# Kernel optimization log

Measured on AMD Instinct MI355X. Metric: run time of the kernel, lower is better.

Reference implementation:

```python
import jax, jax.numpy as jnp
import numpy as np

B, S, E, H, A, D, V, L = 64, 196, 512, 512, 256, 512, 32000, 32
PAD_IDX = 2


def setup_inputs() -> dict:
    key = jax.random.key(0)
    ks = jax.random.split(key, 20)
    sc = 0.02
    return {
        "encoder_out": jax.random.normal(ks[0], (B, S, E), jnp.float32),
        "pooled": jax.random.normal(ks[1], (B, E), jnp.float32),
        "targets": jax.random.randint(ks[2], (B, L), 0, V, jnp.int64),
        "embedding": jax.random.normal(ks[3], (V, D), jnp.float32) * sc,
        "W_enc": jax.random.normal(ks[4], (A, E), jnp.float32) * sc,
        "b_enc": jnp.zeros((A,), jnp.float32),
        "W_dec": jax.random.normal(ks[5], (A, H), jnp.float32) * sc,
        "b_dec": jnp.zeros((A,), jnp.float32),
        "W_score": jax.random.normal(ks[6], (1, A), jnp.float32) * sc,
        "b_score": jnp.zeros((1,), jnp.float32),
        "W_ih": jax.random.normal(ks[7], (3 * H, D + E), jnp.float32) * sc,
        "W_hh": jax.random.normal(ks[8], (3 * H, H), jnp.float32) * sc,
        "b_ih": jnp.zeros((3 * H,), jnp.float32),
        "b_hh": jnp.zeros((3 * H,), jnp.float32),
        "W_out": jax.random.normal(ks[9], (V, H), jnp.float32) * sc,
        "b_out": jnp.zeros((V,), jnp.float32),
        "W_init": jax.random.normal(ks[10], (H, E), jnp.float32) * sc,
        "b_init": jnp.zeros((H,), jnp.float32),
    }


def reference(encoder_out, pooled, targets, embedding, W_enc, b_enc, W_dec,
              b_dec, W_score, b_score, W_ih, W_hh, b_ih, b_hh, W_out, b_out,
              W_init, b_init):
    # padding_idx=2: that embedding row is zero
    emb_tab = embedding.at[PAD_IDX].set(0.0)
    # initial hidden state from pooled features
    h0 = jnp.tanh(pooled @ W_init.T + b_init)              # (B, H)
    # encoder projection is step-invariant; hoist out of the loop
    enc_proj = jnp.einsum('bse,ae->bsa', encoder_out, W_enc) + b_enc  # (B,S,A)
    # teacher forcing (ratio=1.0): inputs are targets[:, :-1]
    tokens = targets[:, :-1].T                              # (L-1, B)

    def step(h, tok):
        embedded = emb_tab[tok]                             # (B, D)
        # Bahdanau attention
        dec_proj = h @ W_dec.T + b_dec                      # (B, A)
        energy = jnp.tanh(enc_proj + dec_proj[:, None, :])  # (B, S, A)
        scores = jnp.einsum('bsa,a->bs', energy, W_score[0]) + b_score[0]
        weights = jax.nn.softmax(scores, axis=1)            # (B, S)
        context = jnp.einsum('bs,bse->be', weights, encoder_out)  # (B, E)
        # GRU cell (PyTorch gate ordering: r, z, n)
        x = jnp.concatenate([embedded, context], axis=1)    # (B, D+E)
        gi = x @ W_ih.T + b_ih                              # (B, 3H)
        gh = h @ W_hh.T + b_hh                              # (B, 3H)
        gi_r, gi_z, gi_n = jnp.split(gi, 3, axis=1)
        gh_r, gh_z, gh_n = jnp.split(gh, 3, axis=1)
        r = jax.nn.sigmoid(gi_r + gh_r)
        z = jax.nn.sigmoid(gi_z + gh_z)
        n = jnp.tanh(gi_n + r * gh_n)
        h_new = (1.0 - z) * n + z * h
        logits = h_new @ W_out.T + b_out                    # (B, V)
        return h_new, logits

    _, logits = jax.lax.scan(step, h0, tokens)              # (L-1, B, V)
    return jnp.transpose(logits, (1, 0, 2))                 # (B, L-1, V)
```

## Files before the change

### kernel.cpp

```cpp
#include <hip/hip_runtime.h>

using bf16x8 = __attribute__((ext_vector_type(8))) short;
using f32x4  = __attribute__((ext_vector_type(4))) float;

__device__ inline float bf2f(unsigned short h){
  union { unsigned int u; float f; } v; v.u = ((unsigned int)h) << 16; return v.f;
}
__device__ inline unsigned short f2b(float x){
  union { float f; unsigned int u; } v; v.f = x;
  unsigned int r = (v.u + 0x7FFFu + ((v.u >> 16) & 1u)) >> 16;
  return (unsigned short)r;
}
__device__ inline float blo(unsigned int u){ union{unsigned int v; float f;} t; t.v = u << 16; return t.f; }
__device__ inline float bhi(unsigned int u){ union{unsigned int v; float f;} t; t.v = u & 0xffff0000u; return t.f; }

__global__ void conv_k(const float* __restrict__ s, unsigned short* __restrict__ d, int n){
  int i = (blockIdx.x * 256 + threadIdx.x) * 4;
  if (i >= n) return;
  float4 v = *(const float4*)(s + i);
  unsigned int p0 = (unsigned int)f2b(v.x) | ((unsigned int)f2b(v.y) << 16);
  unsigned int p1 = (unsigned int)f2b(v.z) | ((unsigned int)f2b(v.w) << 16);
  *(uint2*)(d + i) = make_uint2(p0, p1);
}

__global__ void wdect_k(const float* __restrict__ Wd, unsigned short* __restrict__ o){
  int idx = blockIdx.x * 256 + threadIdx.x;
  int k = idx >> 8, a = idx & 255;
  o[idx] = f2b(Wd[a * 512 + k]);
}

__global__ void embed_k(const int* __restrict__ tgt, const float* __restrict__ emb,
                        unsigned short* __restrict__ out, int n){
  int idx = blockIdx.x * 256 + threadIdx.x;
  if (idx >= n) return;
  int d = idx & 511, m = idx >> 9, t = m >> 6, b = m & 63;
  int tok = tgt[b * 32 + t];
  float v = (tok == 2) ? 0.f : emb[(long)tok * 512 + d];
  out[idx] = f2b(v);
}

#define EPI_PLAIN 0
#define EPI_TANH  1
#define EPI_OUT   2
#define EPI_B16   3

template<int EPI, bool AF32>
__global__ __launch_bounds__(256)
void gemm_bt(const void* __restrict__ Av, int lda,
             const unsigned short* __restrict__ Bp, int ldb,
             const float* __restrict__ bias,
             float* __restrict__ Cf, unsigned short* __restrict__ Cb, int ldc,
             int K,
             int n_split, const void* __restrict__ A2v,
             const unsigned short* __restrict__ B2p, int lda2, int ldb2)
{
  __shared__ __align__(16) unsigned short As[64][40];
  __shared__ __align__(16) unsigned short Bs[256][40];

  int m0 = blockIdx.x * 64;
  int n0 = blockIdx.y * 256;
  const void* Ap = Av; const unsigned short* Bq = Bp;
  int la = lda, lb = ldb, nB = n0;
  if (n_split > 0 && n0 >= n_split){ Ap = A2v; Bq = B2p; la = lda2; lb = ldb2; nB = n0 - n_split; }

  int tid  = threadIdx.x;
  int wave = tid >> 6, lane = tid & 63, quad = lane >> 4, lrow = lane & 15;

  f32x4 acc[4][4];
#pragma unroll
  for (int i = 0; i < 4; ++i)
#pragma unroll
    for (int j = 0; j < 4; ++j)
#pragma unroll
      for (int r = 0; r < 4; ++r) acc[i][j][r] = 0.f;

  int ar = tid >> 2, ac = (tid & 3) * 8;

  for (int k0 = 0; k0 < K; k0 += 32){
    if (AF32){
      const float* A32 = (const float*)Ap;
      const float4* src = (const float4*)(A32 + (long)(m0 + ar) * la + k0 + ac);
      float4 x0 = src[0], x1 = src[1];
      unsigned int p0 = (unsigned int)f2b(x0.x) | ((unsigned int)f2b(x0.y) << 16);
      unsigned int p1 = (unsigned int)f2b(x0.z) | ((unsigned int)f2b(x0.w) << 16);
      unsigned int p2 = (unsigned int)f2b(x1.x) | ((unsigned int)f2b(x1.y) << 16);
      unsigned int p3 = (unsigned int)f2b(x1.z) | ((unsigned int)f2b(x1.w) << 16);
      *(uint4*)&As[ar][ac] = make_uint4(p0, p1, p2, p3);
    } else {
      const unsigned short* A16 = (const unsigned short*)Ap;
      *(uint4*)&As[ar][ac] = *(const uint4*)(A16 + (long)(m0 + ar) * la + k0 + ac);
    }
#pragma unroll
    for (int c = 0; c < 4; ++c){
      int id = tid + c * 256; int br = id >> 2, bc = (id & 3) * 8;
      *(uint4*)&Bs[br][bc] = *(const uint4*)(Bq + (long)(nB + br) * lb + k0 + bc);
    }
    __syncthreads();

    bf16x8 af[4], bfr[4];
#pragma unroll
    for (int mf = 0; mf < 4; ++mf) af[mf]  = *(const bf16x8*)&As[mf * 16 + lrow][quad * 8];
#pragma unroll
    for (int nf = 0; nf < 4; ++nf) bfr[nf] = *(const bf16x8*)&Bs[wave * 64 + nf * 16 + lrow][quad * 8];
#pragma unroll
    for (int mf = 0; mf < 4; ++mf)
#pragma unroll
      for (int nf = 0; nf < 4; ++nf)
        acc[mf][nf] = __builtin_amdgcn_mfma_f32_16x16x32_bf16(af[mf], bfr[nf], acc[mf][nf], 0, 0, 0);
    __syncthreads();
  }

#pragma unroll
  for (int mf = 0; mf < 4; ++mf){
#pragma unroll
    for (int nf = 0; nf < 4; ++nf){
#pragma unroll
      for (int r = 0; r < 4; ++r){
        int m = m0 + mf * 16 + quad * 4 + r;
        int n = n0 + wave * 64 + nf * 16 + lrow;
        float v = acc[mf][nf][r];
        if (bias) v += bias[n];
        if (EPI == EPI_TANH){
          v = tanhf(v);
          Cf[(long)m * ldc + n] = v;
          Cb[(long)m * ldc + n] = f2b(v);
        } else if (EPI == EPI_OUT){
          Cf[(long)(m & 63) * (31 * 32000) + (long)(m >> 6) * 32000 + n] = v;
        } else if (EPI == EPI_B16){
          Cb[(long)m * ldc + n] = f2b(v);
        } else {
          Cf[(long)m * ldc + n] = v;
        }
      }
    }
  }
}

__global__ __launch_bounds__(512)
void attn_step(const uint4* __restrict__ ep4,
               const unsigned int* __restrict__ eo2,
               const float* __restrict__ W_score,
               const float* __restrict__ b_dec,
               const float* __restrict__ b_hh,
               const float* __restrict__ gi_emb,
               const float* __restrict__ giq,
               float* __restrict__ h_all,
               unsigned short* __restrict__ h_b16,
               const uint2* __restrict__ WdecT4,
               unsigned short* __restrict__ ctx_b16,
               int t, int do_gates, int do_attn)
{
  __shared__ __align__(16) uint4 ep_s4[6272];
  __shared__ float sh_h[512];
  __shared__ float2 dpw[256];
  __shared__ float spart[2048];
  __shared__ float sw[256];
  __shared__ float wred[16];

  int b = blockIdx.x, tid = threadIdx.x;
  int lane = tid & 63, wv = tid >> 6;

  float hv;
  if (do_gates){
    int j = tid;
    long ge = ((long)(t - 1) * 64 + b) * 1536;
    long gq = (long)b * 3072;
    float gir = gi_emb[ge + j]        + giq[gq + j];
    float giz = gi_emb[ge + 512 + j]  + giq[gq + 512 + j];
    float gin = gi_emb[ge + 1024 + j] + giq[gq + 1024 + j];
    float ghr = giq[gq + 1536 + j]        + b_hh[j];
    float ghz = giq[gq + 1536 + 512 + j]  + b_hh[512 + j];
    float ghn = giq[gq + 1536 + 1024 + j] + b_hh[1024 + j];
    float rr = 1.f / (1.f + __expf(-(gir + ghr)));
    float zz = 1.f / (1.f + __expf(-(giz + ghz)));
    float nn = tanhf(gin + rr * ghn);
    float hp = h_all[((long)(t - 1) * 64 + b) * 512 + j];
    hv = (1.f - zz) * nn + zz * hp;
    h_all[((long)t * 64 + b) * 512 + j] = hv;
    h_b16[((long)t * 64 + b) * 512 + j] = f2b(hv);
  } else {
    hv = h_all[((long)t * 64 + b) * 512 + tid];
  }
  if (!do_attn) return;

  sh_h[tid] = hv;
  float wsc = (tid < 256) ? W_score[tid] : 0.f;

  {
    const uint4* src = ep4 + (long)b * 6272;
    for (int c = tid; c < 6272; c += 512){
      int r = c >> 5, col = c & 31;
      ep_s4[(r << 5) | (col ^ (r & 7))] = src[c];
    }
  }
  __syncthreads();

  {
    int a4 = tid & 63, kg = tid >> 6;
    const uint2* wp = WdecT4 + ((kg << 12) | a4);
    const float* hp = &sh_h[kg << 6];
    float ac0 = 0.f, ac1 = 0.f, ac2 = 0.f, ac3 = 0.f;
#pragma unroll 16
    for (int kk = 0; kk < 64; ++kk){
      uint2 wq = wp[kk << 6];
      float hk = hp[kk];
      ac0 += hk * blo(wq.x); ac1 += hk * bhi(wq.x);
      ac2 += hk * blo(wq.y); ac3 += hk * bhi(wq.y);
    }
    *(float4*)&spart[(kg << 8) | (a4 << 2)] = make_float4(ac0, ac1, ac2, ac3);
  }
  __syncthreads();
  if (tid < 256){
    float dp = b_dec[tid];
#pragma unroll
    for (int kg = 0; kg < 8; ++kg) dp += spart[(kg << 8) | tid];
    dpw[tid] = make_float2(dp, wsc);
  }
  __syncthreads();

  {
    int s = tid & 255, half = tid >> 8;
    float acc = 0.f;
    if (s < 196){
      int rb = s << 5, sx = s & 7;
#pragma unroll 4
      for (int j = 0; j < 16; ++j){
        uint4 v = ep_s4[rb | (((half << 4) | j) ^ sx)];
        int aj = (half << 7) | (j << 3);
#define SCP(uu, ab) { \
        float2 dA = dpw[ab], dB = dpw[(ab) + 1]; \
        float xA = blo(uu) + dA.x, xB = bhi(uu) + dB.x; \
        float eA = __expf(2.f * xA), eB = __expf(2.f * xB); \
        acc += dA.y * (1.f - 2.f / (eA + 1.f)); \
        acc += dB.y * (1.f - 2.f / (eB + 1.f)); }
        SCP(v.x, aj) SCP(v.y, aj + 2) SCP(v.z, aj + 4) SCP(v.w, aj + 6)
#undef SCP
      }
    }
    spart[tid] = acc;
  }
  __syncthreads();

  float sc = -1e30f, ee = 0.f;
  if (tid < 256) sc = (tid < 196) ? (spart[tid] + spart[tid + 256]) : -1e30f;
  float mm = sc;
#pragma unroll
  for (int off = 32; off >= 1; off >>= 1) mm = fmaxf(mm, __shfl_xor(mm, off));
  if (tid < 256 && lane == 0) wred[wv] = mm;
  __syncthreads();
  float mx = fmaxf(fmaxf(wred[0], wred[1]), fmaxf(wred[2], wred[3]));
  if (tid < 256){
    ee = (tid < 196) ? __expf(sc - mx) : 0.f;
    sw[tid] = ee;
  }
  float ss = ee;
#pragma unroll
  for (int off = 32; off >= 1; off >>= 1) ss += __shfl_xor(ss, off);
  if (tid < 256 && lane == 0) wred[8 + wv] = ss;
  __syncthreads();
  float inv = 1.f / (wred[8] + wred[9] + wred[10] + wred[11]);

  {
    int e2 = tid & 255, sh2 = tid >> 8;
    const unsigned int* src = eo2 + ((long)b * 196 + sh2 * 98) * 256 + e2;
    float a0 = 0.f, a1 = 0.f;
#pragma unroll 2
    for (int s2 = 0; s2 < 98; ++s2){
      unsigned int v = src[(long)s2 * 256];
      float w = sw[sh2 * 98 + s2];
      a0 += w * blo(v); a1 += w * bhi(v);
    }
    *(float2*)&spart[(sh2 << 9) | (e2 << 1)] = make_float2(a0, a1);
  }
  __syncthreads();
  {
    float cv = (spart[tid] + spart[tid + 512]) * inv;
    ctx_b16[(b << 9) | tid] = f2b(cv);
  }
}

extern "C" void kernel_launch(void* const* d_in, const int* in_sizes, int n_in,
                              void* d_out, int out_size, void* d_ws, size_t ws_size,
                              hipStream_t stream)
{
  (void)in_sizes; (void)n_in; (void)out_size; (void)ws_size;
  const float* encoder_out = (const float*)d_in[0];
  const float* pooled      = (const float*)d_in[1];
  const int*   targets     = (const int*)d_in[2];
  const float* embedding   = (const float*)d_in[3];
  const float* W_enc  = (const float*)d_in[4];
  const float* b_enc  = (const float*)d_in[5];
  const float* W_dec  = (const float*)d_in[6];
  const float* b_dec  = (const float*)d_in[7];
  const float* W_score= (const float*)d_in[8];
  const float* W_ih   = (const float*)d_in[10];
  const float* W_hh   = (const float*)d_in[11];
  const float* b_ih   = (const float*)d_in[12];
  const float* b_hh   = (const float*)d_in[13];
  const float* W_out  = (const float*)d_in[14];
  const float* b_out  = (const float*)d_in[15];
  const float* W_init = (const float*)d_in[16];
  const float* b_init = (const float*)d_in[17];
  float* out = (float*)d_out;

  char* w = (char*)d_ws;
  unsigned short* eo_b16  = (unsigned short*)w; w += 12845056;
  float* gi_emb           = (float*)w;          w += 12189696;
  float* h_all            = (float*)w;          w += 4194304;
  unsigned short* h_b16   = (unsigned short*)w; w += 2097152;
  float* giq              = (float*)w;          w += 786432;
  unsigned short* ctx_b16 = (unsigned short*)w; w += 65536;
  unsigned short* emb_b16 = (unsigned short*)w; w += 2031616;
  unsigned short* Wout_b  = (unsigned short*)w; w += 32768000;
  unsigned short* Wih_b   = (unsigned short*)w; w += 3145728;
  unsigned short* Whh_b   = (unsigned short*)w; w += 1572864;
  unsigned short* WdecT_b = (unsigned short*)w; w += 262144;
  unsigned short* Winit_b = (unsigned short*)w; w += 524288;
  unsigned short* Wenc_b  = (unsigned short*)w; w += 262144;
  unsigned short* ep_b16  = (unsigned short*)w; w += 6422528;

  auto conv = [&](const float* s, unsigned short* d, int n){
    conv_k<<<dim3((n / 4 + 255) / 256), dim3(256), 0, stream>>>(s, d, n);
  };
  conv(W_out,  Wout_b,  32000 * 512);
  conv(W_ih,   Wih_b,   1536 * 1024);
  conv(W_hh,   Whh_b,   1536 * 512);
  conv(W_init, Winit_b, 512 * 512);
  conv(W_enc,  Wenc_b,  256 * 512);
  conv(encoder_out, eo_b16, 64 * 196 * 512);
  wdect_k<<<dim3(512), dim3(256), 0, stream>>>(W_dec, WdecT_b);
  embed_k<<<dim3((1984 * 512) / 256), dim3(256), 0, stream>>>(targets, embedding, emb_b16, 1984 * 512);

  gemm_bt<EPI_TANH, true><<<dim3(1, 2), 256, 0, stream>>>(
      pooled, 512, Winit_b, 512, b_init, h_all, h_b16, 512, 512, 0, nullptr, nullptr, 0, 0);
  gemm_bt<EPI_B16, true><<<dim3(196, 1), 256, 0, stream>>>(
      encoder_out, 512, Wenc_b, 512, b_enc, nullptr, ep_b16, 256, 512, 0, nullptr, nullptr, 0, 0);
  gemm_bt<EPI_PLAIN, false><<<dim3(31, 6), 256, 0, stream>>>(
      emb_b16, 512, Wih_b, 1024, b_ih, gi_emb, nullptr, 1536, 512, 0, nullptr, nullptr, 0, 0);

  for (int t = 0; t < 31; ++t){
    attn_step<<<dim3(64), dim3(512), 0, stream>>>(
        (const uint4*)ep_b16, (const unsigned int*)eo_b16, W_score, b_dec, b_hh,
        gi_emb, giq, h_all, h_b16, (const uint2*)WdecT_b, ctx_b16,
        t, (t > 0) ? 1 : 0, 1);
    gemm_bt<EPI_PLAIN, false><<<dim3(1, 12), 256, 0, stream>>>(
        ctx_b16, 512, Wih_b + 512, 1024, nullptr, giq, nullptr, 3072, 512,
        1536, h_b16 + (long)t * 64 * 512, Whh_b, 512, 512);
  }
  attn_step<<<dim3(64), dim3(512), 0, stream>>>(
      (const uint4*)ep_b16, (const unsigned int*)eo_b16, W_score, b_dec, b_hh,
      gi_emb, giq, h_all, h_b16, (const uint2*)WdecT_b, ctx_b16, 31, 1, 0);

  gemm_bt<EPI_OUT, false><<<dim3(31, 125), 256, 0, stream>>>(
      h_b16 + 64 * 512, 512, Wout_b, 512, b_out, out, nullptr, 0, 512,
      0, nullptr, nullptr, 0, 0);
}
```

Before: 2.167 ms.

## Fuse recurrent GRU loop into one persistent per-batch kernel with MFMA gate GEMV

The 31 per-step attention launches plus per-step gate GEMM launches are replaced by a single persistent kernel with one block per batch row that loops over all time steps. Encoder projections stay in LDS, and the GRU hidden state and gate pre-activations are kept on chip. The ctx·W_ih and h·W_hh products are computed inside the block with MFMA 16x16x32 bf16 instructions, using weights pre-swizzled into fragment order by a new wfrag kernel. This removes about 62 launches and the global round trips between them. The cost is that only 64 blocks run, and each block now streams the full 3 MB of gate weights every step while the MFMA A operand is padded from one row to sixteen.

```diff
diff --git a/kernel.cpp b/kernel.cpp
--- a/kernel.cpp
+++ b/kernel.cpp
@@ -27,6 +27,15 @@
   int idx = blockIdx.x * 256 + threadIdx.x;
   int k = idx >> 8, a = idx & 255;
   o[idx] = f2b(Wd[a * 512 + k]);
+}
+
+__global__ void wfrag_k(const float* __restrict__ src, int ld, int koff,
+                        unsigned short* __restrict__ dst){
+  int d = blockIdx.x * 256 + threadIdx.x;
+  int j = d & 7, lane = (d >> 3) & 63, kit = (d >> 9) & 15, nt = d >> 13;
+  int n = nt * 16 + (lane & 15);
+  int k = kit * 32 + ((lane >> 4) << 3) + j;
+  dst[d] = f2b(src[(long)n * ld + koff + k]);
 }
 
 __global__ void embed_k(const int* __restrict__ tgt, const float* __restrict__ emb,
@@ -137,54 +146,34 @@
 }
 
 __global__ __launch_bounds__(512)
-void attn_step(const uint4* __restrict__ ep4,
-               const unsigned int* __restrict__ eo2,
-               const float* __restrict__ W_score,
-               const float* __restrict__ b_dec,
-               const float* __restrict__ b_hh,
-               const float* __restrict__ gi_emb,
-               const float* __restrict__ giq,
-               float* __restrict__ h_all,
-               unsigned short* __restrict__ h_b16,
-               const uint2* __restrict__ WdecT4,
-               unsigned short* __restrict__ ctx_b16,
-               int t, int do_gates, int do_attn)
+void loop_k(const uint4* __restrict__ ep4,
+            const unsigned int* __restrict__ eo2,
+            const float* __restrict__ W_score,
+            const float* __restrict__ b_dec,
+            const float* __restrict__ b_hh,
+            const float* __restrict__ gi_emb,
+            const float* __restrict__ h0_all,
+            unsigned short* __restrict__ h_b16,
+            const uint2* __restrict__ WdecT4,
+            const unsigned short* __restrict__ Wihf,
+            const unsigned short* __restrict__ Whhf)
 {
   __shared__ __align__(16) uint4 ep_s4[6272];
   __shared__ float sh_h[512];
+  __shared__ unsigned short sh_hb[512];
+  __shared__ unsigned short sh_cb[512];
   __shared__ float2 dpw[256];
   __shared__ float spart[2048];
   __shared__ float sw[256];
   __shared__ float wred[16];
+  __shared__ float giq_lds[3072];
 
   int b = blockIdx.x, tid = threadIdx.x;
-  int lane = tid & 63, wv = tid >> 6;
-
-  float hv;
-  if (do_gates){
-    int j = tid;
-    long ge = ((long)(t - 1) * 64 + b) * 1536;
-    long gq = (long)b * 3072;
-    float gir = gi_emb[ge + j]        + giq[gq + j];
-    float giz = gi_emb[ge + 512 + j]  + giq[gq + 512 + j];
-    float gin = gi_emb[ge + 1024 + j] + giq[gq + 1024 + j];
-    float ghr = giq[gq + 1536 + j]        + b_hh[j];
-    float ghz = giq[gq + 1536 + 512 + j]  + b_hh[512 + j];
-    float ghn = giq[gq + 1536 + 1024 + j] + b_hh[1024 + j];
-    float rr = 1.f / (1.f + __expf(-(gir + ghr)));
-    float zz = 1.f / (1.f + __expf(-(giz + ghz)));
-    float nn = tanhf(gin + rr * ghn);
-    float hp = h_all[((long)(t - 1) * 64 + b) * 512 + j];
-    hv = (1.f - zz) * nn + zz * hp;
-    h_all[((long)t * 64 + b) * 512 + j] = hv;
-    h_b16[((long)t * 64 + b) * 512 + j] = f2b(hv);
-  } else {
-    hv = h_all[((long)t * 64 + b) * 512 + tid];
-  }
-  if (!do_attn) return;
-
-  sh_h[tid] = hv;
-  float wsc = (tid < 256) ? W_score[tid] : 0.f;
+  int lane = tid & 63, wv = tid >> 6, quad = lane >> 4, lrow = lane & 15;
+
+  float wsc  = (tid < 256) ? W_score[tid] : 0.f;
+  float bdec = (tid < 256) ? b_dec[tid] : 0.f;
+  float bhh0 = b_hh[tid], bhh1 = b_hh[512 + tid], bhh2 = b_hh[1024 + tid];
 
   {
     const uint4* src = ep4 + (long)b * 6272;
@@ -193,89 +182,142 @@
       ep_s4[(r << 5) | (col ^ (r & 7))] = src[c];
     }
   }
-  __syncthreads();
-
-  {
-    int a4 = tid & 63, kg = tid >> 6;
-    const uint2* wp = WdecT4 + ((kg << 12) | a4);
-    const float* hp = &sh_h[kg << 6];
-    float ac0 = 0.f, ac1 = 0.f, ac2 = 0.f, ac3 = 0.f;
+
+  float h_prev = 0.f;
+
+  for (int t = 0; t <= 31; ++t){
+    float hv;
+    if (t > 0){
+      int j = tid;
+      long ge = ((long)(t - 1) * 64 + b) * 1536;
+      float gir = gi_emb[ge + j]        + giq_lds[j];
+      float giz = gi_emb[ge + 512 + j]  + giq_lds[512 + j];
+      float gin = gi_emb[ge + 1024 + j] + giq_lds[1024 + j];
+      float ghr = giq_lds[1536 + j] + bhh0;
+      float ghz = giq_lds[2048 + j] + bhh1;
+      float ghn = giq_lds[2560 + j] + bhh2;
+      float rr = 1.f / (1.f + __expf(-(gir + ghr)));
+      float zz = 1.f / (1.f + __expf(-(giz + ghz)));
+      float nn = tanhf(gin + rr * ghn);
+      hv = (1.f - zz) * nn + zz * h_prev;
+      h_b16[((long)t * 64 + b) * 512 + j] = f2b(hv);
+    } else {
+      hv = h0_all[(long)b * 512 + tid];
+    }
+    h_prev = hv;
+    if (t == 31) break;
+
+    sh_h[tid] = hv;
+    sh_hb[tid] = f2b(hv);
+    __syncthreads();
+
+    {
+      int a4 = tid & 63, kg = tid >> 6;
+      const uint2* wp = WdecT4 + ((kg << 12) | a4);
+      const float* hp = &sh_h[kg << 6];
+      float ac0 = 0.f, ac1 = 0.f, ac2 = 0.f, ac3 = 0.f;
 #pragma unroll 16
-    for (int kk = 0; kk < 64; ++kk){
-      uint2 wq = wp[kk << 6];
-      float hk = hp[kk];
-      ac0 += hk * blo(wq.x); ac1 += hk * bhi(wq.x);
-      ac2 += hk * blo(wq.y); ac3 += hk * bhi(wq.y);
-    }
-    *(float4*)&spart[(kg << 8) | (a4 << 2)] = make_float4(ac0, ac1, ac2, ac3);
-  }
-  __syncthreads();
-  if (tid < 256){
-    float dp = b_dec[tid];
-#pragma unroll
-    for (int kg = 0; kg < 8; ++kg) dp += spart[(kg << 8) | tid];
-    dpw[tid] = make_float2(dp, wsc);
-  }
-  __syncthreads();
-
-  {
-    int s = tid & 255, half = tid >> 8;
-    float acc = 0.f;
-    if (s < 196){
-      int rb = s << 5, sx = s & 7;
+      for (int kk = 0; kk < 64; ++kk){
+        uint2 wq = wp[kk << 6];
+        float hk = hp[kk];
+        ac0 += hk * blo(wq.x); ac1 += hk * bhi(wq.x);
+        ac2 += hk * blo(wq.y); ac3 += hk * bhi(wq.y);
+      }
+      *(float4*)&spart[(kg << 8) | (a4 << 2)] = make_float4(ac0, ac1, ac2, ac3);
+    }
+    __syncthreads();
+    if (tid < 256){
+      float dp = bdec;
+#pragma unroll
+      for (int kg = 0; kg < 8; ++kg) dp += spart[(kg << 8) | tid];
+      dpw[tid] = make_float2(dp, wsc);
+    }
+    __syncthreads();
+
+    {
+      int s = tid & 255, half = tid >> 8;
+      float acc = 0.f;
+      if (s < 196){
+        int rb = s << 5, sx = s & 7;
 #pragma unroll 4
-      for (int j = 0; j < 16; ++j){
-        uint4 v = ep_s4[rb | (((half << 4) | j) ^ sx)];
-        int aj = (half << 7) | (j << 3);
+        for (int j = 0; j < 16; ++j){
+          uint4 v = ep_s4[rb | (((half << 4) | j) ^ sx)];
+          int aj = (half << 7) | (j << 3);
 #define SCP(uu, ab) { \
-        float2 dA = dpw[ab], dB = dpw[(ab) + 1]; \
-        float xA = blo(uu) + dA.x, xB = bhi(uu) + dB.x; \
-        float eA = __expf(2.f * xA), eB = __expf(2.f * xB); \
-        acc += dA.y * (1.f - 2.f / (eA + 1.f)); \
-        acc += dB.y * (1.f - 2.f / (eB + 1.f)); }
-        SCP(v.x, aj) SCP(v.y, aj + 2) SCP(v.z, aj + 4) SCP(v.w, aj + 6)
+          float2 dA = dpw[ab], dB = dpw[(ab) + 1]; \
+          float xA = blo(uu) + dA.x, xB = bhi(uu) + dB.x; \
+          float eA = __expf(2.f * xA), eB = __expf(2.f * xB); \
+          acc += dA.y * (1.f - 2.f / (eA + 1.f)); \
+          acc += dB.y * (1.f - 2.f / (eB + 1.f)); }
+          SCP(v.x, aj) SCP(v.y, aj + 2) SCP(v.z, aj + 4) SCP(v.w, aj + 6)
 #undef SCP
-      }
-    }
-    spart[tid] = acc;
-  }
-  __syncthreads();
-
-  float sc = -1e30f, ee = 0.f;
-  if (tid < 256) sc = (tid < 196) ? (spart[tid] + spart[tid + 256]) : -1e30f;
-  float mm = sc;
-#pragma unroll
-  for (int off = 32; off >= 1; off >>= 1) mm = fmaxf(mm, __shfl_xor(mm, off));
-  if (tid < 256 && lane == 0) wred[wv] = mm;
-  __syncthreads();
-  float mx = fmaxf(fmaxf(wred[0], wred[1]), fmaxf(wred[2], wred[3]));
-  if (tid < 256){
-    ee = (tid < 196) ? __expf(sc - mx) : 0.f;
-    sw[tid] = ee;
-  }
-  float ss = ee;
-#pragma unroll
-  for (int off = 32; off >= 1; off >>= 1) ss += __shfl_xor(ss, off);
-  if (tid < 256 && lane == 0) wred[8 + wv] = ss;
-  __syncthreads();
-  float inv = 1.f / (wred[8] + wred[9] + wred[10] + wred[11]);
-
-  {
-    int e2 = tid & 255, sh2 = tid >> 8;
-    const unsigned int* src = eo2 + ((long)b * 196 + sh2 * 98) * 256 + e2;
-    float a0 = 0.f, a1 = 0.f;
+        }
+      }
+      spart[tid] = acc;
+    }
+    __syncthreads();
+
+    float sc = -1e30f, ee = 0.f;
+    if (tid < 256) sc = (tid < 196) ? (spart[tid] + spart[tid + 256]) : -1e30f;
+    float mm = sc;
+#pragma unroll
+    for (int off = 32; off >= 1; off >>= 1) mm = fmaxf(mm, __shfl_xor(mm, off));
+    if (tid < 256 && lane == 0) wred[wv] = mm;
+    __syncthreads();
+    float mx = fmaxf(fmaxf(wred[0], wred[1]), fmaxf(wred[2], wred[3]));
+    if (tid < 256){
+      ee = (tid < 196) ? __expf(sc - mx) : 0.f;
+      sw[tid] = ee;
+    }
+    float ss = ee;
+#pragma unroll
+    for (int off = 32; off >= 1; off >>= 1) ss += __shfl_xor(ss, off);
+    if (tid < 256 && lane == 0) wred[8 + wv] = ss;
+    __syncthreads();
+    float inv = 1.f / (wred[8] + wred[9] + wred[10] + wred[11]);
+
+    {
+      int e2 = tid & 255, sh2 = tid >> 8;
+      const unsigned int* src = eo2 + ((long)b * 196 + sh2 * 98) * 256 + e2;
+      float a0 = 0.f, a1 = 0.f;
 #pragma unroll 2
-    for (int s2 = 0; s2 < 98; ++s2){
-      unsigned int v = src[(long)s2 * 256];
-      float w = sw[sh2 * 98 + s2];
-      a0 += w * blo(v); a1 += w * bhi(v);
-    }
-    *(float2*)&spart[(sh2 << 9) | (e2 << 1)] = make_float2(a0, a1);
-  }
-  __syncthreads();
-  {
-    float cv = (spart[tid] + spart[tid + 512]) * inv;
-    ctx_b16[(b << 9) | tid] = f2b(cv);
+      for (int s2 = 0; s2 < 98; ++s2){
+        unsigned int v = src[(long)s2 * 256];
+        float w = sw[sh2 * 98 + s2];
+        a0 += w * blo(v); a1 += w * bhi(v);
+      }
+      *(float2*)&spart[(sh2 << 9) | (e2 << 1)] = make_float2(a0, a1);
+    }
+    __syncthreads();
+    sh_cb[tid] = f2b((spart[tid] + spart[tid + 512]) * inv);
+    __syncthreads();
+
+    {
+      const unsigned short* asrc = (wv < 4) ? sh_cb : sh_hb;
+      uint4 af[16];
+#pragma unroll
+      for (int kit = 0; kit < 16; ++kit){
+        uint4 av = *(const uint4*)&asrc[(kit << 5) + (quad << 3)];
+        if (lrow) av = make_uint4(0, 0, 0, 0);
+        af[kit] = av;
+      }
+      const unsigned short* wsrc = (wv < 4) ? Wihf : Whhf;
+      int tbase = (wv & 3) * 24;
+      int obase = (wv < 4) ? 0 : 1536;
+      for (int i = 0; i < 24; ++i){
+        int tl = tbase + i;
+        const unsigned short* wb = wsrc + ((long)tl << 13) + (size_t)lane * 8;
+        f32x4 a4 = {0.f, 0.f, 0.f, 0.f};
+#pragma unroll
+        for (int kit = 0; kit < 16; ++kit){
+          bf16x8 bfrag = *(const bf16x8*)(wb + (kit << 9));
+          bf16x8 afr; *(uint4*)&afr = af[kit];
+          a4 = __builtin_amdgcn_mfma_f32_16x16x32_bf16(afr, bfrag, a4, 0, 0, 0);
+        }
+        if (lane < 16) giq_lds[obase + tl * 16 + lane] = a4[0];
+      }
+    }
+    __syncthreads();
   }
 }
 
@@ -306,17 +348,16 @@
   char* w = (char*)d_ws;
   unsigned short* eo_b16  = (unsigned short*)w; w += 12845056;
   float* gi_emb           = (float*)w;          w += 12189696;
-  float* h_all            = (float*)w;          w += 4194304;
+  float* h_all            = (float*)w;          w += 131072;
   unsigned short* h_b16   = (unsigned short*)w; w += 2097152;
-  float* giq              = (float*)w;          w += 786432;
-  unsigned short* ctx_b16 = (unsigned short*)w; w += 65536;
   unsigned short* emb_b16 = (unsigned short*)w; w += 2031616;
   unsigned short* Wout_b  = (unsigned short*)w; w += 32768000;
   unsigned short* Wih_b   = (unsigned short*)w; w += 3145728;
-  unsigned short* Whh_b   = (unsigned short*)w; w += 1572864;
   unsigned short* WdecT_b = (unsigned short*)w; w += 262144;
   unsigned short* Winit_b = (unsigned short*)w; w += 524288;
   unsigned short* Wenc_b  = (unsigned short*)w; w += 262144;
+  unsigned short* Wihf_b  = (unsigned short*)w; w += 1572864;
+  unsigned short* Whhf_b  = (unsigned short*)w; w += 1572864;
   unsigned short* ep_b16  = (unsigned short*)w; w += 6422528;
 
   auto conv = [&](const float* s, unsigned short* d, int n){
@@ -324,11 +365,12 @@
   };
   conv(W_out,  Wout_b,  32000 * 512);
   conv(W_ih,   Wih_b,   1536 * 1024);
-  conv(W_hh,   Whh_b,   1536 * 512);
   conv(W_init, Winit_b, 512 * 512);
   conv(W_enc,  Wenc_b,  256 * 512);
   conv(encoder_out, eo_b16, 64 * 196 * 512);
   wdect_k<<<dim3(512), dim3(256), 0, stream>>>(W_dec, WdecT_b);
+  wfrag_k<<<dim3(3072), dim3(256), 0, stream>>>(W_ih, 1024, 512, Wihf_b);
+  wfrag_k<<<dim3(3072), dim3(256), 0, stream>>>(W_hh, 512, 0, Whhf_b);
   embed_k<<<dim3((1984 * 512) / 256), dim3(256), 0, stream>>>(targets, embedding, emb_b16, 1984 * 512);
 
   gemm_bt<EPI_TANH, true><<<dim3(1, 2), 256, 0, stream>>>(
@@ -338,18 +380,9 @@
   gemm_bt<EPI_PLAIN, false><<<dim3(31, 6), 256, 0, stream>>>(
       emb_b16, 512, Wih_b, 1024, b_ih, gi_emb, nullptr, 1536, 512, 0, nullptr, nullptr, 0, 0);
 
-  for (int t = 0; t < 31; ++t){
-    attn_step<<<dim3(64), dim3(512), 0, stream>>>(
-        (const uint4*)ep_b16, (const unsigned int*)eo_b16, W_score, b_dec, b_hh,
-        gi_emb, giq, h_all, h_b16, (const uint2*)WdecT_b, ctx_b16,
-        t, (t > 0) ? 1 : 0, 1);
-    gemm_bt<EPI_PLAIN, false><<<dim3(1, 12), 256, 0, stream>>>(
-        ctx_b16, 512, Wih_b + 512, 1024, nullptr, giq, nullptr, 3072, 512,
-        1536, h_b16 + (long)t * 64 * 512, Whh_b, 512, 512);
-  }
-  attn_step<<<dim3(64), dim3(512), 0, stream>>>(
+  loop_k<<<dim3(64), dim3(512), 0, stream>>>(
       (const uint4*)ep_b16, (const unsigned int*)eo_b16, W_score, b_dec, b_hh,
-      gi_emb, giq, h_all, h_b16, (const uint2*)WdecT_b, ctx_b16, 31, 1, 0);
+      gi_emb, h_all, h_b16, (const uint2*)WdecT_b, Wihf_b, Whhf_b);
 
   gemm_bt<EPI_OUT, false><<<dim3(31, 125), 256, 0, stream>>>(
       h_b16 + 64 * 512, 512, Wout_b, 512, b_out, out, nullptr, 0, 512,
```

New measurement: 5.819 ms. +168.6%, slower.
